# Kernel tuning notes

Hardware: AMD Instinct MI355X
Metric: run time of the kernel (lower is better)

The kernel has to match this reference:

```python
import jax, jax.numpy as jnp
import numpy as np

NUM_Q_HEADS = 32
NUM_KV_HEADS = 8
HEAD_DIM = 128
HIDDEN = 4096
MAX_WAVELENGTH = 10000.0
ROPE_SCALING = 1.0


def apply_rope(x, start_index=0):
    # x: [b, s, h, d]; keras_hub RotaryEmbedding: concat-half (NeoX/Llama) style
    s, d = x.shape[1], x.shape[3]
    inv_freq = 1.0 / (MAX_WAVELENGTH ** (jnp.arange(0, d, 2, dtype=jnp.float32) / d))
    pos = (jnp.arange(s, dtype=jnp.float32) + start_index) / ROPE_SCALING
    freq = pos[:, None] * inv_freq[None, :]           # [s, d/2]
    emb = jnp.concatenate([freq, freq], axis=-1)      # [s, d]
    cos = jnp.cos(emb)[None, :, None, :]
    sin = jnp.sin(emb)[None, :, None, :]
    x1, x2 = jnp.split(x, 2, axis=-1)
    half_rot = jnp.concatenate([-x2, x1], axis=-1)
    return x * cos + half_rot * sin


def setup_inputs() -> dict:
    key = jax.random.key(0)
    k1, k2, k3, k4, k5 = jax.random.split(key, 5)
    B, S = 1, 2048
    hidden_states = jax.random.normal(k1, (B, S, HIDDEN), dtype=jnp.float32)
    # causal mask [B, q, k]
    attention_mask = jnp.broadcast_to(jnp.tril(jnp.ones((S, S), dtype=bool)), (B, S, S))
    scale = 1.0 / np.sqrt(HIDDEN)
    wq = jax.random.normal(k2, (HIDDEN, NUM_Q_HEADS, HEAD_DIM), dtype=jnp.float32) * scale
    wk = jax.random.normal(k3, (HIDDEN, NUM_KV_HEADS, HEAD_DIM), dtype=jnp.float32) * scale
    wv = jax.random.normal(k4, (HIDDEN, NUM_KV_HEADS, HEAD_DIM), dtype=jnp.float32) * scale
    wo = jax.random.normal(k5, (NUM_Q_HEADS, HEAD_DIM, HIDDEN), dtype=jnp.float32) * scale
    return {"hidden_states": hidden_states, "attention_mask": attention_mask,
            "wq": wq, "wk": wk, "wv": wv, "wo": wo}


def reference(hidden_states, attention_mask, wq, wk, wv, wo):
    groups = NUM_Q_HEADS // NUM_KV_HEADS
    norm = jnp.sqrt(jnp.asarray(HEAD_DIM, dtype=hidden_states.dtype))
    query = jnp.einsum('bqm,muh->bquh', hidden_states, wq)   # [b,q,Hq,d]
    key = jnp.einsum('bkm,mvh->bkvh', hidden_states, wk)     # [b,k,Hkv,d]
    value = jnp.einsum('bkm,mvh->bkvh', hidden_states, wv)
    query = apply_rope(query)
    key = apply_rope(key)
    # repeat KV heads for GQA (ops.repeat on head axis)
    key = jnp.repeat(key, groups, axis=2)
    value = jnp.repeat(value, groups, axis=2)
    scores = jnp.einsum('bquh,bkuh->buqk', query, key) / norm  # [b,H,q,k]
    scores = scores.astype(jnp.float32)
    scores = jnp.where(attention_mask[:, None, :, :], scores, jnp.float32(-1e9))
    probs = jax.nn.softmax(scores, axis=-1).astype(hidden_states.dtype)
    attn = jnp.einsum('buqk,bkuh->bquh', probs, value)
    out = jnp.einsum('bquh,uhm->bqm', attn, wo)
    return out
```

## Files before the change

kernel.cpp:

```cpp
#include <hip/hip_runtime.h>
#include <hip/hip_bf16.h>
#include <stdint.h>

#define S_LEN 2048
#define HID 4096
#define NQH 32
#define NKVH 8
#define HD 128
#define QKV_LD 6144

typedef __attribute__((ext_vector_type(8))) short bf16x8;
typedef __attribute__((ext_vector_type(4))) float f32x4;
typedef __attribute__((address_space(3))) uint8_t lds_u8_t;
typedef __attribute__((address_space(1))) uint8_t glb_u8_t;

__device__ __forceinline__ void g2lds16(const void* g, void* l) {
  __builtin_amdgcn_global_load_lds((const glb_u8_t*)g, (lds_u8_t*)l, 16, 0, 0);
}

__device__ __forceinline__ ushort f2bf(float x) {
  return __builtin_bit_cast(ushort, __float2bfloat16(x));
}
__device__ __forceinline__ float bf2f(ushort x) {
  return __bfloat162float(__builtin_bit_cast(__hip_bfloat16, x));
}

__global__ void k_f32_to_bf16(const float* __restrict__ in, ushort* __restrict__ out, int n4) {
  int i = blockIdx.x * blockDim.x + threadIdx.x;
  if (i >= n4) return;
  float4 v = ((const float4*)in)[i];
  ushort4 o;
  o.x = f2bf(v.x); o.y = f2bf(v.y); o.z = f2bf(v.z); o.w = f2bf(v.w);
  ((ushort4*)out)[i] = o;
}

__global__ void k_transpose_f32_bf16(const float* __restrict__ in, ushort* __restrict__ out,
                                     int ldi, int ldo) {
  __shared__ float tile[32][33];
  int j0 = blockIdx.x * 32, i0 = blockIdx.y * 32;
  int tx = threadIdx.x, ty = threadIdx.y;
#pragma unroll
  for (int k = 0; k < 4; ++k)
    tile[ty + 8 * k][tx] = in[(size_t)(i0 + ty + 8 * k) * ldi + j0 + tx];
  __syncthreads();
#pragma unroll
  for (int k = 0; k < 4; ++k)
    out[(size_t)(j0 + ty + 8 * k) * ldo + i0 + tx] = f2bf(tile[tx][ty + 8 * k]);
}

__global__ void k_transpose_bf16_head(const ushort* __restrict__ in, ushort* __restrict__ out) {
  __shared__ ushort tile[32][33];
  int hkv = blockIdx.z;
  int j0 = blockIdx.x * 32;
  int i0 = blockIdx.y * 32;
  const ushort* ih = in + hkv * HD;
  ushort* oh = out + (size_t)hkv * HD * S_LEN;
  int tx = threadIdx.x, ty = threadIdx.y;
#pragma unroll
  for (int k = 0; k < 4; ++k)
    tile[ty + 8 * k][tx] = ih[(size_t)(i0 + ty + 8 * k) * QKV_LD + j0 + tx];
  __syncthreads();
#pragma unroll
  for (int k = 0; k < 4; ++k)
    oh[(size_t)(j0 + ty + 8 * k) * S_LEN + i0 + tx] = tile[tx][ty + 8 * k];
}

__global__ void k_rope(ushort* __restrict__ X, int H, int logH, int ld, float mul) {
  int t = blockIdx.x * 256 + threadIdx.x;
  int d = t & 63;
  int rest = t >> 6;
  int h = rest & (H - 1);
  int s = rest >> logH;
  size_t base = (size_t)s * ld + h * HD + d;
  float inv = exp2f(-(float)d * 0.20762050593046014f);
  float fr = (float)s * inv;
  float c = cosf(fr), sn = sinf(fr);
  float x1 = bf2f(X[base]);
  float x2 = bf2f(X[base + 64]);
  X[base]      = f2bf((x1 * c - x2 * sn) * mul);
  X[base + 64] = f2bf((x2 * c + x1 * sn) * mul);
}

template <int OUT_BF16>
__global__ __launch_bounds__(256) void k_gemm_bt(const ushort* __restrict__ A,
                                                 const ushort* __restrict__ BT,
                                                 void* __restrict__ Cv, int K, int ldc) {
  __shared__ ushort As[128 * 64];
  __shared__ ushort Bs[128 * 64];
  int tid = threadIdx.x;
  int lane = tid & 63, wave = tid >> 6;
  int hi = lane >> 4, lo = lane & 15;
  int wr = wave >> 1, wc = wave & 1;
  int m0 = blockIdx.y * 128, n0 = blockIdx.x * 128;
  const f32x4 z4 = {0.f, 0.f, 0.f, 0.f};
  f32x4 acc[4][4];
#pragma unroll
  for (int i = 0; i < 4; ++i)
#pragma unroll
    for (int j = 0; j < 4; ++j) acc[i][j] = z4;

  const char* Ab = (const char*)A;
  const char* Bb = (const char*)BT;
  for (int k0 = 0; k0 < K; k0 += 64) {
#pragma unroll
    for (int j = 0; j < 4; ++j) {
      int L = wave * 4096 + j * 1024 + lane * 16;
      int row = L >> 7, colb = L & 127;
      g2lds16(Ab + ((size_t)(m0 + row) * K + k0) * 2 + colb, (char*)As + wave * 4096 + j * 1024);
      g2lds16(Bb + ((size_t)(n0 + row) * K + k0) * 2 + colb, (char*)Bs + wave * 4096 + j * 1024);
    }
    __syncthreads();
#pragma unroll
    for (int kk = 0; kk < 2; ++kk) {
      bf16x8 af[4], bfr[4];
#pragma unroll
      for (int i = 0; i < 4; ++i) {
        af[i] = *(const bf16x8*)((const char*)As + (64 * wr + 16 * i + lo) * 128 + kk * 64 + hi * 16);
        bfr[i] = *(const bf16x8*)((const char*)Bs + (64 * wc + 16 * i + lo) * 128 + kk * 64 + hi * 16);
      }
#pragma unroll
      for (int mi = 0; mi < 4; ++mi)
#pragma unroll
        for (int ni = 0; ni < 4; ++ni)
          acc[mi][ni] = __builtin_amdgcn_mfma_f32_16x16x32_bf16(af[mi], bfr[ni], acc[mi][ni], 0, 0, 0);
    }
    __syncthreads();
  }
#pragma unroll
  for (int mi = 0; mi < 4; ++mi)
#pragma unroll
    for (int ni = 0; ni < 4; ++ni)
#pragma unroll
      for (int r = 0; r < 4; ++r) {
        int row = m0 + 64 * wr + 16 * mi + 4 * hi + r;
        int col = n0 + 64 * wc + 16 * ni + lo;
        if (OUT_BF16) {
          ((ushort*)Cv)[(size_t)row * ldc + col] = f2bf(acc[mi][ni][r]);
        } else {
          ((float*)Cv)[(size_t)row * ldc + col] = acc[mi][ni][r];
        }
      }
}

__global__ __launch_bounds__(256) void k_attn(const ushort* __restrict__ Q,
                                              const ushort* __restrict__ Kg,
                                              const ushort* __restrict__ VT,
                                              ushort* __restrict__ Ob) {
  __shared__ char smem[2 * 16384 + 2 * 16384 + 9216];
  int tid = threadIdx.x, lane = tid & 63, wave = tid >> 6;
  int hi = lane >> 4, lo = lane & 15;
  int h = blockIdx.y;
  int hkv = h >> 2;
  char* Pw = smem + 65536 + wave * 2304;
  const f32x4 z4 = {0.f, 0.f, 0.f, 0.f};
  bf16x8 ones;
#pragma unroll
  for (int i = 0; i < 8; ++i) ones[i] = (short)0x3F80;

  int L = wave * 4096 + lane * 16;
  int krow0 = L >> 8, kcolb = L & 255;
  int vrow0 = L >> 7, vcolb = L & 127;

#pragma unroll 1
  for (int pp = 0; pp < 2; ++pp) {
    int qt = pp == 0 ? (int)blockIdx.x : 31 - (int)blockIdx.x;
    int q0 = qt * 64;

    bf16x8 qf[4];
    const char* qrow = (const char*)Q + ((size_t)(q0 + 16 * wave + lo) * QKV_LD + h * HD) * 2;
#pragma unroll
    for (int c = 0; c < 4; ++c) qf[c] = *(const bf16x8*)(qrow + c * 64 + hi * 16);

    f32x4 oacc[8];
#pragma unroll
    for (int dg = 0; dg < 8; ++dg) oacc[dg] = z4;
    f32x4 lacc = z4;

#pragma unroll
    for (int j = 0; j < 4; ++j) {
      int kr = krow0 + j * 4, vr = vrow0 + j * 8;
      int ksrc = kcolb ^ ((kr & 7) << 4);
      int vsrc = vcolb ^ ((vr & 7) << 4);
      g2lds16((const char*)Kg + ((size_t)kr * QKV_LD + hkv * HD) * 2 + ksrc,
              smem + wave * 4096 + j * 1024);
      g2lds16((const char*)VT + ((size_t)(hkv * HD + vr) * S_LEN) * 2 + vsrc,
              smem + 32768 + wave * 4096 + j * 1024);
    }
    __syncthreads();

    for (int t = 0; t <= qt; ++t) {
      int cur = t & 1;
      char* Ks = smem + cur * 16384;
      char* Vs = smem + 32768 + cur * 16384;
      if (t < qt) {
        int kv1 = (t + 1) * 64;
        char* Kn = smem + (cur ^ 1) * 16384;
        char* Vn = smem + 32768 + (cur ^ 1) * 16384;
#pragma unroll
        for (int j = 0; j < 4; ++j) {
          int kr = krow0 + j * 4, vr = vrow0 + j * 8;
          int ksrc = kcolb ^ ((kr & 7) << 4);
          int vsrc = vcolb ^ ((vr & 7) << 4);
          g2lds16((const char*)Kg + ((size_t)(kv1 + kr) * QKV_LD + hkv * HD) * 2 + ksrc,
                  Kn + wave * 4096 + j * 1024);
          g2lds16((const char*)VT + ((size_t)(hkv * HD + vr) * S_LEN + kv1) * 2 + vsrc,
                  Vn + wave * 4096 + j * 1024);
        }
      }
      int kv0 = t * 64;

      f32x4 sg[4];
#pragma unroll
      for (int g = 0; g < 4; ++g) {
        f32x4 s = z4;
#pragma unroll
        for (int c = 0; c < 4; ++c) {
          int row = 16 * g + lo;
          int cb = (c * 64 + hi * 16) ^ ((row & 7) << 4);
          bf16x8 kf = *(const bf16x8*)(Ks + row * 256 + cb);
          s = __builtin_amdgcn_mfma_f32_16x16x32_bf16(qf[c], kf, s, 0, 0, 0);
        }
        sg[g] = s;
      }

      float pvv[4][4];
      if (t < qt) {
#pragma unroll
        for (int g = 0; g < 4; ++g)
#pragma unroll
          for (int r = 0; r < 4; ++r) pvv[g][r] = exp2f(sg[g][r]);
      } else {
#pragma unroll
        for (int g = 0; g < 4; ++g) {
          int kv_idx = kv0 + 16 * g + lo;
#pragma unroll
          for (int r = 0; r < 4; ++r) {
            int q_idx = q0 + 16 * wave + 4 * hi + r;
            float v = sg[g][r];
            if (kv_idx > q_idx) v = -1e30f;
            pvv[g][r] = exp2f(v);
          }
        }
      }

      {
        ushort* Pu = (ushort*)Pw;
#pragma unroll
        for (int g = 0; g < 4; ++g)
#pragma unroll
          for (int r = 0; r < 4; ++r)
            Pu[(4 * hi + r) * 72 + 16 * g + lo] = f2bf(pvv[g][r]);
      }
      asm volatile("" ::: "memory");

      bf16x8 pa[2];
#pragma unroll
      for (int c2 = 0; c2 < 2; ++c2)
        pa[c2] = *(const bf16x8*)(Pw + lo * 144 + c2 * 64 + hi * 16);
#pragma unroll
      for (int c2 = 0; c2 < 2; ++c2)
        lacc = __builtin_amdgcn_mfma_f32_16x16x32_bf16(pa[c2], ones, lacc, 0, 0, 0);
#pragma unroll
      for (int dg = 0; dg < 8; ++dg) {
#pragma unroll
        for (int c2 = 0; c2 < 2; ++c2) {
          int row = 16 * dg + lo;
          int cb = (c2 * 64 + hi * 16) ^ ((row & 7) << 4);
          bf16x8 vf = *(const bf16x8*)(Vs + row * 128 + cb);
          oacc[dg] = __builtin_amdgcn_mfma_f32_16x16x32_bf16(pa[c2], vf, oacc[dg], 0, 0, 0);
        }
      }
      __syncthreads();
    }

#pragma unroll
    for (int r = 0; r < 4; ++r) {
      float inv_l = 1.0f / lacc[r];
      int q = q0 + 16 * wave + 4 * hi + r;
      ushort* orow = Ob + (size_t)q * HID + h * HD;
#pragma unroll
      for (int dg = 0; dg < 8; ++dg)
        orow[16 * dg + lo] = f2bf(oacc[dg][r] * inv_l);
    }
  }
}

extern "C" void kernel_launch(void* const* d_in, const int* in_sizes, int n_in,
                              void* d_out, int out_size, void* d_ws, size_t ws_size,
                              hipStream_t stream) {
  const float* hidden = (const float*)d_in[0];
  const float* wq = (const float*)d_in[2];
  const float* wk = (const float*)d_in[3];
  const float* wv = (const float*)d_in[4];
  const float* wo = (const float*)d_in[5];

  char* ws = (char*)d_ws;
  ushort* hid_bf = (ushort*)(ws);
  ushort* wqkvT  = (ushort*)(ws + 16777216);
  ushort* VT     = (ushort*)(ws + 67108864);

  ushort* QKV = (ushort*)d_out;
  float* out = (float*)d_out;

  const float qmul = (float)(0.08838834764831845 * 1.4426950408889634);

  dim3 tb(32, 8);
  k_f32_to_bf16<<<8192, 256, 0, stream>>>(hidden, hid_bf, 2097152);
  k_transpose_f32_bf16<<<dim3(128, 128), tb, 0, stream>>>(wq, wqkvT, 4096, 4096);
  k_transpose_f32_bf16<<<dim3(32, 128), tb, 0, stream>>>(wk, wqkvT + (size_t)4096 * 4096, 1024, 4096);
  k_transpose_f32_bf16<<<dim3(32, 128), tb, 0, stream>>>(wv, wqkvT + (size_t)5120 * 4096, 1024, 4096);
  k_gemm_bt<1><<<dim3(48, 16), 256, 0, stream>>>(hid_bf, wqkvT, (void*)QKV, 4096, QKV_LD);
  k_rope<<<16384, 256, 0, stream>>>(QKV, 32, 5, QKV_LD, qmul);
  k_rope<<<4096, 256, 0, stream>>>(QKV + 4096, 8, 3, QKV_LD, 1.0f);
  k_transpose_bf16_head<<<dim3(4, 64, 8), tb, 0, stream>>>(QKV + 5120, VT);
  k_transpose_f32_bf16<<<dim3(128, 128), tb, 0, stream>>>(wo, wqkvT, 4096, 4096);
  k_attn<<<dim3(16, 32), 256, 0, stream>>>(QKV, QKV + 4096, VT, hid_bf);
  k_gemm_bt<0><<<dim3(32, 16), 256, 0, stream>>>(hid_bf, wqkvT, (void*)out, 4096, 4096);
}
```

Baseline: 573.6 us.

## Replace GEMM with 256x256-tile, 4-stage pipelined, swizzled-LDS bf16 MFMA kernel

Both projection GEMMs now use a new kernel with 256x256 output tiles and 512 threads. It runs a 4-buffer LDS ring fed by async global-to-LDS loads kept three k-steps ahead, with explicit vmcnt waits and one barrier per step. This replaces the old synchronous load-then-compute loop that had two barriers per step. An XOR swizzle on LDS columns is meant to avoid bank conflicts, and setprio raises priority around the MFMA bursts. In exchange, the grids are much smaller (192 and 128 blocks), which may underfill the 256 CUs. The kernel also uses 128KB of LDS and heavy register pressure.

```diff
diff --git a/kernel.cpp b/kernel.cpp
--- a/kernel.cpp
+++ b/kernel.cpp
@@ -23,6 +23,12 @@
 }
 __device__ __forceinline__ float bf2f(ushort x) {
   return __bfloat162float(__builtin_bit_cast(__hip_bfloat16, x));
+}
+
+__device__ __forceinline__ void hard_barrier() {
+  __builtin_amdgcn_sched_barrier(0);
+  __builtin_amdgcn_s_barrier();
+  __builtin_amdgcn_sched_barrier(0);
 }
 
 __global__ void k_f32_to_bf16(const float* __restrict__ in, ushort* __restrict__ out, int n4) {
@@ -82,62 +88,104 @@
 }
 
 template <int OUT_BF16>
-__global__ __launch_bounds__(256) void k_gemm_bt(const ushort* __restrict__ A,
-                                                 const ushort* __restrict__ BT,
-                                                 void* __restrict__ Cv, int K, int ldc) {
-  __shared__ ushort As[128 * 64];
-  __shared__ ushort Bs[128 * 64];
-  int tid = threadIdx.x;
-  int lane = tid & 63, wave = tid >> 6;
-  int hi = lane >> 4, lo = lane & 15;
-  int wr = wave >> 1, wc = wave & 1;
-  int m0 = blockIdx.y * 128, n0 = blockIdx.x * 128;
-  const f32x4 z4 = {0.f, 0.f, 0.f, 0.f};
-  f32x4 acc[4][4];
-#pragma unroll
-  for (int i = 0; i < 4; ++i)
-#pragma unroll
-    for (int j = 0; j < 4; ++j) acc[i][j] = z4;
+__global__ __launch_bounds__(512, 2) void k_gemm256(const ushort* __restrict__ A,
+                                                    const ushort* __restrict__ BT,
+                                                    void* __restrict__ Cv, int K, int ldc) {
+  __shared__ char smem[131072];
+  const int tid = threadIdx.x;
+  const int lane = tid & 63, wave = tid >> 6;
+  const int lo = lane & 15, hi = lane >> 4;
+  const int wm = wave >> 2, wn = wave & 3;
+  const int m0 = blockIdx.y * 256, n0 = blockIdx.x * 256;
+  const int NT = K >> 5;
+
+  const int src_cb = (((lane & 3) ^ ((lane >> 2) & 3)) << 4);
+  const int rd_cb = ((hi ^ (lo & 3)) << 4);
+  const int srow = wave * 16 + (lane >> 2);
 
   const char* Ab = (const char*)A;
   const char* Bb = (const char*)BT;
-  for (int k0 = 0; k0 < K; k0 += 64) {
-#pragma unroll
-    for (int j = 0; j < 4; ++j) {
-      int L = wave * 4096 + j * 1024 + lane * 16;
-      int row = L >> 7, colb = L & 127;
-      g2lds16(Ab + ((size_t)(m0 + row) * K + k0) * 2 + colb, (char*)As + wave * 4096 + j * 1024);
-      g2lds16(Bb + ((size_t)(n0 + row) * K + k0) * 2 + colb, (char*)Bs + wave * 4096 + j * 1024);
+
+  const f32x4 z4 = {0.f, 0.f, 0.f, 0.f};
+  f32x4 acc[8][4];
+#pragma unroll
+  for (int m = 0; m < 8; ++m)
+#pragma unroll
+    for (int n = 0; n < 4; ++n) acc[m][n] = z4;
+
+  auto burst = [&](int u) {
+    char* base = smem + (u & 3) * 32768;
+    size_t k0b = (size_t)(u << 5) * 2;
+#pragma unroll
+    for (int i = 0; i < 2; ++i) {
+      int r = srow + i * 128;
+      g2lds16(Ab + (size_t)(m0 + r) * K * 2 + k0b + src_cb, base + i * 8192 + wave * 1024);
+      g2lds16(Bb + (size_t)(n0 + r) * K * 2 + k0b + src_cb, base + 16384 + i * 8192 + wave * 1024);
     }
-    __syncthreads();
-#pragma unroll
-    for (int kk = 0; kk < 2; ++kk) {
-      bf16x8 af[4], bfr[4];
-#pragma unroll
-      for (int i = 0; i < 4; ++i) {
-        af[i] = *(const bf16x8*)((const char*)As + (64 * wr + 16 * i + lo) * 128 + kk * 64 + hi * 16);
-        bfr[i] = *(const bf16x8*)((const char*)Bs + (64 * wc + 16 * i + lo) * 128 + kk * 64 + hi * 16);
-      }
-#pragma unroll
-      for (int mi = 0; mi < 4; ++mi)
-#pragma unroll
-        for (int ni = 0; ni < 4; ++ni)
-          acc[mi][ni] = __builtin_amdgcn_mfma_f32_16x16x32_bf16(af[mi], bfr[ni], acc[mi][ni], 0, 0, 0);
-    }
-    __syncthreads();
+  };
+
+  auto step = [&](int j) {
+    const char* SA = smem + (j & 3) * 32768;
+    const char* SB = SA + 16384;
+    bf16x8 a[8], b[4];
+#pragma unroll
+    for (int m = 0; m < 4; ++m)
+      a[m] = *(const bf16x8*)(SA + (wm * 128 + m * 16 + lo) * 64 + rd_cb);
+#pragma unroll
+    for (int n = 0; n < 4; ++n)
+      b[n] = *(const bf16x8*)(SB + (wn * 64 + n * 16 + lo) * 64 + rd_cb);
+    __builtin_amdgcn_s_setprio(1);
+#pragma unroll
+    for (int m = 0; m < 4; ++m)
+#pragma unroll
+      for (int n = 0; n < 4; ++n)
+        acc[m][n] = __builtin_amdgcn_mfma_f32_16x16x32_bf16(a[m], b[n], acc[m][n], 0, 0, 0);
+    __builtin_amdgcn_s_setprio(0);
+#pragma unroll
+    for (int m = 4; m < 8; ++m)
+      a[m] = *(const bf16x8*)(SA + (wm * 128 + m * 16 + lo) * 64 + rd_cb);
+    __builtin_amdgcn_s_setprio(1);
+#pragma unroll
+    for (int m = 4; m < 8; ++m)
+#pragma unroll
+      for (int n = 0; n < 4; ++n)
+        acc[m][n] = __builtin_amdgcn_mfma_f32_16x16x32_bf16(a[m], b[n], acc[m][n], 0, 0, 0);
+    __builtin_amdgcn_s_setprio(0);
+  };
+
+  burst(0); burst(1); burst(2);
+  asm volatile("s_waitcnt vmcnt(8)" ::: "memory");
+  hard_barrier();
+
+  int j = 0;
+  for (; j < NT - 3; ++j) {
+    burst(j + 3);
+    step(j);
+    asm volatile("s_waitcnt vmcnt(8)" ::: "memory");
+    hard_barrier();
   }
-#pragma unroll
-  for (int mi = 0; mi < 4; ++mi)
-#pragma unroll
-    for (int ni = 0; ni < 4; ++ni)
+  step(j);
+  asm volatile("s_waitcnt vmcnt(4)" ::: "memory");
+  hard_barrier();
+  ++j;
+  step(j);
+  asm volatile("s_waitcnt vmcnt(0)" ::: "memory");
+  hard_barrier();
+  ++j;
+  step(j);
+
+#pragma unroll
+  for (int m = 0; m < 8; ++m)
+#pragma unroll
+    for (int n = 0; n < 4; ++n)
 #pragma unroll
       for (int r = 0; r < 4; ++r) {
-        int row = m0 + 64 * wr + 16 * mi + 4 * hi + r;
-        int col = n0 + 64 * wc + 16 * ni + lo;
+        int row = m0 + wm * 128 + m * 16 + 4 * hi + r;
+        int col = n0 + wn * 64 + n * 16 + lo;
         if (OUT_BF16) {
-          ((ushort*)Cv)[(size_t)row * ldc + col] = f2bf(acc[mi][ni][r]);
+          ((ushort*)Cv)[(size_t)row * ldc + col] = f2bf(acc[m][n][r]);
         } else {
-          ((float*)Cv)[(size_t)row * ldc + col] = acc[mi][ni][r];
+          ((float*)Cv)[(size_t)row * ldc + col] = acc[m][n][r];
         }
       }
 }
@@ -309,11 +357,11 @@
   k_transpose_f32_bf16<<<dim3(128, 128), tb, 0, stream>>>(wq, wqkvT, 4096, 4096);
   k_transpose_f32_bf16<<<dim3(32, 128), tb, 0, stream>>>(wk, wqkvT + (size_t)4096 * 4096, 1024, 4096);
   k_transpose_f32_bf16<<<dim3(32, 128), tb, 0, stream>>>(wv, wqkvT + (size_t)5120 * 4096, 1024, 4096);
-  k_gemm_bt<1><<<dim3(48, 16), 256, 0, stream>>>(hid_bf, wqkvT, (void*)QKV, 4096, QKV_LD);
+  k_gemm256<1><<<dim3(24, 8), 512, 0, stream>>>(hid_bf, wqkvT, (void*)QKV, 4096, QKV_LD);
   k_rope<<<16384, 256, 0, stream>>>(QKV, 32, 5, QKV_LD, qmul);
   k_rope<<<4096, 256, 0, stream>>>(QKV + 4096, 8, 3, QKV_LD, 1.0f);
   k_transpose_bf16_head<<<dim3(4, 64, 8), tb, 0, stream>>>(QKV + 5120, VT);
   k_transpose_f32_bf16<<<dim3(128, 128), tb, 0, stream>>>(wo, wqkvT, 4096, 4096);
   k_attn<<<dim3(16, 32), 256, 0, stream>>>(QKV, QKV + 4096, VT, hid_bf);
-  k_gemm_bt<0><<<dim3(32, 16), 256, 0, stream>>>(hid_bf, wqkvT, (void*)out, 4096, 4096);
-}
+  k_gemm256<0><<<dim3(16, 8), 512, 0, stream>>>(hid_bf, wqkvT, (void*)out, 4096, 4096);
+}
```

Measured after the change: 513.1 us. 1.12x faster.
